# Kernel tuning notes

Hardware: AMD Instinct MI355X
Metric: run time of the kernel (lower is better)

The kernel has to match this reference:

```python
import jax, jax.numpy as jnp
import numpy as np

EPS = 1e-7


def ciou_pairwise(b1, b2):
    # b1: (N,1,4), b2: (1,N,4) in xyxy; returns (N,N) CIoU
    b1x1, b1y1, b1x2, b1y2 = b1[..., 0], b1[..., 1], b1[..., 2], b1[..., 3]
    b2x1, b2y1, b2x2, b2y2 = b2[..., 0], b2[..., 1], b2[..., 2], b2[..., 3]

    # intersection
    iw = jnp.clip(jnp.minimum(b1x2, b2x2) - jnp.maximum(b1x1, b2x1), 0.0)
    ih = jnp.clip(jnp.minimum(b1y2, b2y2) - jnp.maximum(b1y1, b2y1), 0.0)
    inter = iw * ih

    w1, h1 = b1x2 - b1x1, b1y2 - b1y1
    w2, h2 = b2x2 - b2x1, b2y2 - b2y1
    union = w1 * h1 + w2 * h2 - inter + EPS
    iou = inter / union

    # smallest enclosing box diagonal
    cw = jnp.maximum(b1x2, b2x2) - jnp.minimum(b1x1, b2x1)
    ch = jnp.maximum(b1y2, b2y2) - jnp.minimum(b1y1, b2y1)
    c2 = cw * cw + ch * ch + EPS

    # squared center distance
    rho2 = ((b2x1 + b2x2 - b1x1 - b1x2) ** 2 + (b2y1 + b2y2 - b1y1 - b1y2) ** 2) / 4.0

    # aspect-ratio consistency term
    v = (4.0 / (np.pi ** 2)) * (jnp.arctan(w2 / (h2 + EPS)) - jnp.arctan(w1 / (h1 + EPS))) ** 2
    alpha = jax.lax.stop_gradient(v / (v - iou + (1.0 + EPS)))
    return iou - (rho2 / c2 + v * alpha)


def setup_inputs() -> dict:
    key = jax.random.key(0)
    k1, k2, k3 = jax.random.split(key, 3)
    N = 4096
    conf = jax.random.uniform(k1, (N, 1), dtype=jnp.float32)           # confidence in [0,1)
    xy1 = jax.random.uniform(k2, (N, 2), dtype=jnp.float32) * 600.0    # top-left corner
    wh = jax.random.uniform(k3, (N, 2), dtype=jnp.float32) * 100.0 + 1.0  # width/height >= 1
    x = jnp.concatenate([conf, xy1, xy1 + wh], axis=1)                 # (N, 5): conf, x1, y1, x2, y2
    gamma = jnp.zeros((1,), dtype=jnp.float32)
    return {"x": x, "gamma": gamma}


def reference(x, gamma):
    boxes = x[:, 1:]
    conf = x[:, 0]
    iou = ciou_pairwise(boxes[:, None, :], boxes[None, :, :])          # (N, N)
    conf_matrix = conf[:, None] * conf[None, :]                        # (N, N) outer product
    attention = jax.nn.softmax(iou * conf_matrix, axis=-1)             # (N, N)
    x_prime = x * gamma + attention @ x                                # (N, 5)
    return jax.nn.sigmoid(x_prime)
```

## Files before the change

### kernel.cpp

```cpp
#include <hip/hip_runtime.h>
#include <math.h>

#define N 4096
#define FEPS 1e-7f
#define HEPS 5e-8f
#define BLK 256
#define JT 64
#define CH 64
#define NPAIR (CH / 2)
#define N6 (N * 6)
#define KATAN 0.6366197723675814f
#define SQL2E 1.2011224087864498f

typedef float v2f __attribute__((ext_vector_type(2)));


__global__ void feat_kernel(const float* __restrict__ x,
                            float* __restrict__ feat_row,
                            float* __restrict__ feat_pair) {
    int i = blockIdx.x * blockDim.x + threadIdx.x;
    if (i >= N) return;
    float cf = x[i * 5 + 0], x1 = x[i * 5 + 1], y1 = x[i * 5 + 2];
    float x2 = x[i * 5 + 3], y2 = x[i * 5 + 4];
    float w = x2 - x1, h = y2 - y1;
    float rec[12];
    rec[0] = x1; rec[1] = y1; rec[2] = x2; rec[3] = y2;
    rec[4] = (x1 + x2) * 0.5f; rec[5] = (y1 + y2) * 0.5f;
    rec[6] = w; rec[7] = h;
    rec[8] = fmaf(w, h, HEPS);
    rec[9] = KATAN * atanf(w / (h + FEPS));
    rec[10] = cf * SQL2E; rec[11] = cf;
    float4* dr = (float4*)(feat_row + (size_t)i * 12);
    dr[0] = make_float4(rec[0], rec[1], rec[2], rec[3]);
    dr[1] = make_float4(rec[4], rec[5], rec[6], rec[7]);
    dr[2] = make_float4(rec[8], rec[9], rec[10], rec[11]);
    float* dp = feat_pair + (size_t)(i >> 1) * 24 + (i & 1);
#pragma unroll
    for (int k = 0; k < 12; k++) dp[k * 2] = rec[k];
}

__device__ __forceinline__ v2f min2(v2f a, v2f b) {
    v2f r; r.x = fminf(a.x, b.x); r.y = fminf(a.y, b.y); return r;
}
__device__ __forceinline__ v2f max2(v2f a, v2f b) {
    v2f r; r.x = fmaxf(a.x, b.x); r.y = fmaxf(a.y, b.y); return r;
}
__device__ __forceinline__ v2f rcp2(v2f a) {
    v2f r; r.x = __builtin_amdgcn_rcpf(a.x); r.y = __builtin_amdgcn_rcpf(a.y); return r;
}
__device__ __forceinline__ v2f exp22(v2f a) {
    v2f r; r.x = __builtin_amdgcn_exp2f(a.x); r.y = __builtin_amdgcn_exp2f(a.y); return r;
}

__global__ __launch_bounds__(BLK) void ciou_attn_kernel(
        const float* __restrict__ feat_row,
        const float* __restrict__ feat_pair,
        float* __restrict__ part) {
    __shared__ float jrec[NPAIR * 24];
    const int tid = threadIdx.x;
    const int gb = blockIdx.x / JT;
    const int jt = blockIdx.x % JT;
    const int i = gb * BLK + tid;

    if (tid < 192) {
        ((float4*)jrec)[tid] =
            ((const float4*)(feat_pair + (size_t)jt * NPAIR * 24))[tid];
    }

    const float4* rp = (const float4*)(feat_row + (size_t)i * 12);
    const float4 r0 = rp[0], r1 = rp[1], r2 = rp[2];
    const float rx1 = r0.x, ry1 = r0.y, rx2 = r0.z, ry2 = r0.w;
    const float rhx = r1.x, rhy = r1.y, rw = r1.z, rh = r1.w;
    const float rareps = r2.x, rat = r2.y, rcf2 = r2.z;

    __syncthreads();

    v2f sum = 0.f, a0 = 0.f, a1 = 0.f, a2 = 0.f, a3 = 0.f, a4 = 0.f;
    const float ONEP = 1.f + FEPS;

#pragma unroll 4
    for (int p = 0; p < NPAIR; p++) {
        const float* f = &jrec[p * 24];
        const v2f X1 = *(const v2f*)(f + 0),  Y1 = *(const v2f*)(f + 2);
        const v2f X2 = *(const v2f*)(f + 4),  Y2 = *(const v2f*)(f + 6);
        const v2f HX = *(const v2f*)(f + 8),  HY = *(const v2f*)(f + 10);
        const v2f W  = *(const v2f*)(f + 12), H  = *(const v2f*)(f + 14);
        const v2f AR = *(const v2f*)(f + 16), AT = *(const v2f*)(f + 18);
        const v2f CF2 = *(const v2f*)(f + 20), CF = *(const v2f*)(f + 22);

        v2f iwr = min2(rx2, X2) - max2(rx1, X1);
        v2f ihr = min2(ry2, Y2) - max2(ry1, Y1);
        v2f inter = max2(iwr, 0.f) * max2(ihr, 0.f);
        v2f uni = (rareps + AR) - inter;
        v2f cw = (rw + W) - iwr;
        v2f chh = (rh + H) - ihr;
        v2f c2 = cw * cw + chh * chh + FEPS;
        v2f dx = HX - rhx;
        v2f dy = HY - rhy;
        v2f rho2 = dx * dx + dy * dy;
        v2f da = AT - rat;
        v2f v = da * da;
        v2f P = (v + ONEP) * uni - inter;
        P = max2(P, 1e-12f);
        v2f rr = rcp2(uni * c2 * P);
        v2f t1 = inter * c2 - rho2 * uni;
        v2f vu = v * uni;
        v2f num = t1 * P - (vu * vu) * c2;
        v2f e = exp22((num * rr) * (rcf2 * CF2));
        sum += e;
        a0 += e * CF;
        a1 += e * X1;
        a2 += e * Y1;
        a3 += e * X2;
        a4 += e * Y2;
    }

    float* pp = part + (size_t)jt * N6 + (size_t)i * 6;
    pp[0] = sum.x + sum.y;
    pp[1] = a0.x + a0.y;
    pp[2] = a1.x + a1.y;
    pp[3] = a2.x + a2.y;
    pp[4] = a3.x + a3.y;
    pp[5] = a4.x + a4.y;
}

__global__ void epilogue_kernel(const float* __restrict__ x,
                                const float* __restrict__ gamma,
                                const float* __restrict__ part,
                                float* __restrict__ out) {
    int idx = blockIdx.x * blockDim.x + threadIdx.x;
    if (idx >= N * 5) return;
    int i = idx / 5, c = idx % 5;
    float se = 0.f, a = 0.f;
    const float* p = part + (size_t)i * 6;
#pragma unroll 8
    for (int jt = 0; jt < JT; jt++) {
        se += p[jt * (size_t)N6 + 0];
        a  += p[jt * (size_t)N6 + 1 + c];
    }
    float xp = x[idx] * gamma[0] + a / se;
    out[idx] = 1.f / (1.f + expf(-xp));
}

extern "C" void kernel_launch(void* const* d_in, const int* in_sizes, int n_in,
                              void* d_out, int out_size, void* d_ws, size_t ws_size,
                              hipStream_t stream) {
    const float* x = (const float*)d_in[0];
    const float* gamma = (const float*)d_in[1];
    float* out = (float*)d_out;
    float* part = (float*)d_ws;
    float* feat_row = part + (size_t)JT * N6;
    float* feat_pair = feat_row + (size_t)N * 12;

    feat_kernel<<<(N + BLK - 1) / BLK, BLK, 0, stream>>>(x, feat_row, feat_pair);
    ciou_attn_kernel<<<(N / BLK) * JT, BLK, 0, stream>>>(feat_row, feat_pair, part);
    epilogue_kernel<<<(N * 5 + 255) / 256, 256, 0, stream>>>(x, gamma, part, out);
}
```

Before: 83.47 us.

## Fuse box feature precompute into attention kernel and transpose partials layout

```diff
diff --git a/kernel.cpp b/kernel.cpp
--- a/kernel.cpp
+++ b/kernel.cpp
@@ -8,36 +8,11 @@
 #define JT 64
 #define CH 64
 #define NPAIR (CH / 2)
-#define N6 (N * 6)
 #define KATAN 0.6366197723675814f
 #define SQL2E 1.2011224087864498f
 
 typedef float v2f __attribute__((ext_vector_type(2)));
 
-
-__global__ void feat_kernel(const float* __restrict__ x,
-                            float* __restrict__ feat_row,
-                            float* __restrict__ feat_pair) {
-    int i = blockIdx.x * blockDim.x + threadIdx.x;
-    if (i >= N) return;
-    float cf = x[i * 5 + 0], x1 = x[i * 5 + 1], y1 = x[i * 5 + 2];
-    float x2 = x[i * 5 + 3], y2 = x[i * 5 + 4];
-    float w = x2 - x1, h = y2 - y1;
-    float rec[12];
-    rec[0] = x1; rec[1] = y1; rec[2] = x2; rec[3] = y2;
-    rec[4] = (x1 + x2) * 0.5f; rec[5] = (y1 + y2) * 0.5f;
-    rec[6] = w; rec[7] = h;
-    rec[8] = fmaf(w, h, HEPS);
-    rec[9] = KATAN * atanf(w / (h + FEPS));
-    rec[10] = cf * SQL2E; rec[11] = cf;
-    float4* dr = (float4*)(feat_row + (size_t)i * 12);
-    dr[0] = make_float4(rec[0], rec[1], rec[2], rec[3]);
-    dr[1] = make_float4(rec[4], rec[5], rec[6], rec[7]);
-    dr[2] = make_float4(rec[8], rec[9], rec[10], rec[11]);
-    float* dp = feat_pair + (size_t)(i >> 1) * 24 + (i & 1);
-#pragma unroll
-    for (int k = 0; k < 12; k++) dp[k * 2] = rec[k];
-}
 
 __device__ __forceinline__ v2f min2(v2f a, v2f b) {
     v2f r; r.x = fminf(a.x, b.x); r.y = fminf(a.y, b.y); return r;
@@ -53,8 +28,7 @@
 }
 
 __global__ __launch_bounds__(BLK) void ciou_attn_kernel(
-        const float* __restrict__ feat_row,
-        const float* __restrict__ feat_pair,
+        const float* __restrict__ x,
         float* __restrict__ part) {
     __shared__ float jrec[NPAIR * 24];
     const int tid = threadIdx.x;
@@ -62,16 +36,28 @@
     const int jt = blockIdx.x % JT;
     const int i = gb * BLK + tid;
 
-    if (tid < 192) {
-        ((float4*)jrec)[tid] =
-            ((const float4*)(feat_pair + (size_t)jt * NPAIR * 24))[tid];
+    if (tid < CH) {
+        int j = jt * CH + tid;
+        float cf = x[j * 5 + 0], jx1 = x[j * 5 + 1], jy1 = x[j * 5 + 2];
+        float jx2 = x[j * 5 + 3], jy2 = x[j * 5 + 4];
+        float w = jx2 - jx1, h = jy2 - jy1;
+        float* dp = &jrec[(tid >> 1) * 24 + (tid & 1)];
+        dp[0]  = jx1;               dp[2]  = jy1;
+        dp[4]  = jx2;               dp[6]  = jy2;
+        dp[8]  = (jx1 + jx2) * 0.5f; dp[10] = (jy1 + jy2) * 0.5f;
+        dp[12] = w;                 dp[14] = h;
+        dp[16] = fmaf(w, h, HEPS);
+        dp[18] = KATAN * atanf(w / (h + FEPS));
+        dp[20] = cf * SQL2E;        dp[22] = cf;
     }
 
-    const float4* rp = (const float4*)(feat_row + (size_t)i * 12);
-    const float4 r0 = rp[0], r1 = rp[1], r2 = rp[2];
-    const float rx1 = r0.x, ry1 = r0.y, rx2 = r0.z, ry2 = r0.w;
-    const float rhx = r1.x, rhy = r1.y, rw = r1.z, rh = r1.w;
-    const float rareps = r2.x, rat = r2.y, rcf2 = r2.z;
+    const float rx1 = x[i * 5 + 1], ry1 = x[i * 5 + 2];
+    const float rx2 = x[i * 5 + 3], ry2 = x[i * 5 + 4];
+    const float rw = rx2 - rx1, rh = ry2 - ry1;
+    const float rhx = (rx1 + rx2) * 0.5f, rhy = (ry1 + ry2) * 0.5f;
+    const float rareps = fmaf(rw, rh, HEPS);
+    const float rat = KATAN * atanf(rw / (rh + FEPS));
+    const float rcf2 = x[i * 5 + 0] * SQL2E;
 
     __syncthreads();
 
@@ -115,13 +101,13 @@
         a4 += e * Y2;
     }
 
-    float* pp = part + (size_t)jt * N6 + (size_t)i * 6;
-    pp[0] = sum.x + sum.y;
-    pp[1] = a0.x + a0.y;
-    pp[2] = a1.x + a1.y;
-    pp[3] = a2.x + a2.y;
-    pp[4] = a3.x + a3.y;
-    pp[5] = a4.x + a4.y;
+    float* p = part + (size_t)jt * 6 * N;
+    p[0 * N + i] = sum.x + sum.y;
+    p[1 * N + i] = a0.x + a0.y;
+    p[2 * N + i] = a1.x + a1.y;
+    p[3 * N + i] = a2.x + a2.y;
+    p[4 * N + i] = a3.x + a3.y;
+    p[5 * N + i] = a4.x + a4.y;
 }
 
 __global__ void epilogue_kernel(const float* __restrict__ x,
@@ -130,16 +116,16 @@
                                 float* __restrict__ out) {
     int idx = blockIdx.x * blockDim.x + threadIdx.x;
     if (idx >= N * 5) return;
-    int i = idx / 5, c = idx % 5;
+    int c = idx / N, i = idx - c * N;
     float se = 0.f, a = 0.f;
-    const float* p = part + (size_t)i * 6;
 #pragma unroll 8
     for (int jt = 0; jt < JT; jt++) {
-        se += p[jt * (size_t)N6 + 0];
-        a  += p[jt * (size_t)N6 + 1 + c];
+        const float* p = part + (size_t)jt * 6 * N;
+        se += p[0 * N + i];
+        a  += p[(1 + c) * N + i];
     }
-    float xp = x[idx] * gamma[0] + a / se;
-    out[idx] = 1.f / (1.f + expf(-xp));
+    float xp = x[i * 5 + c] * gamma[0] + a / se;
+    out[i * 5 + c] = 1.f / (1.f + expf(-xp));
 }
 
 extern "C" void kernel_launch(void* const* d_in, const int* in_sizes, int n_in,
@@ -149,10 +135,7 @@
     const float* gamma = (const float*)d_in[1];
     float* out = (float*)d_out;
     float* part = (float*)d_ws;
-    float* feat_row = part + (size_t)JT * N6;
-    float* feat_pair = feat_row + (size_t)N * 12;
 
-    feat_kernel<<<(N + BLK - 1) / BLK, BLK, 0, stream>>>(x, feat_row, feat_pair);
-    ciou_attn_kernel<<<(N / BLK) * JT, BLK, 0, stream>>>(feat_row, feat_pair, part);
+    ciou_attn_kernel<<<(N / BLK) * JT, BLK, 0, stream>>>(x, part);
     epilogue_kernel<<<(N * 5 + 255) / 256, 256, 0, stream>>>(x, gamma, part, out);
 }
```

After: 81.27 us. -2.6%, faster.
